# Performance work log

Measured on AMD Instinct MI355X. Metric: run time of the kernel, lower is better.

The kernel has to match this reference:

```python
import jax, jax.numpy as jnp
import numpy as np

HIDDEN = 1024
HEADS = 16
HEAD_DIM = HIDDEN // HEADS

def setup_inputs() -> dict:
    key = jax.random.key(0)
    ks = jax.random.split(key, 11)
    B, T, D = 2, 2048, HIDDEN
    s = 1.0 / np.sqrt(D)
    return {
        "query": jax.random.normal(ks[0], (B, T, D), jnp.float32),
        "key": jax.random.normal(ks[1], (B, T, D), jnp.float32),
        "value": jax.random.normal(ks[2], (B, T, D), jnp.float32),
        "Wq": jax.random.normal(ks[3], (D, D), jnp.float32) * s,
        "bq": jnp.zeros((D,), jnp.float32),
        "Wk": jax.random.normal(ks[4], (D, D), jnp.float32) * s,
        "bk": jnp.zeros((D,), jnp.float32),
        "Wv": jax.random.normal(ks[5], (D, D), jnp.float32) * s,
        "bv": jnp.zeros((D,), jnp.float32),
        "Wo": jax.random.normal(ks[6], (D, D), jnp.float32) * s,
        "bo": jnp.zeros((D,), jnp.float32),
    }

def reference(query, key, value, Wq, bq, Wk, bk, Wv, bv, Wo, bo):
    B, Tq, D = query.shape
    Tk = key.shape[1]
    H, Hd = HEADS, HEAD_DIM
    # projections -> [B, H, T, Hd]
    Q = (query @ Wq + bq).reshape(B, Tq, H, Hd).transpose(0, 2, 1, 3)
    K = (key @ Wk + bk).reshape(B, Tk, H, Hd).transpose(0, 2, 1, 3)
    V = (value @ Wv + bv).reshape(B, Tk, H, Hd).transpose(0, 2, 1, 3)
    scale = jnp.sqrt(jnp.asarray(Hd, Q.dtype))
    scores = jnp.einsum('bhqd,bhkd->bhqk', Q, K) / scale  # [B,H,Tq,Tk]
    causal = jnp.triu(jnp.ones((Tq, Tk), bool), k=1)
    scores = jnp.where(causal[None, None], jnp.asarray(-jnp.inf, scores.dtype), scores)
    attn = jax.nn.softmax(scores, axis=-1)
    out = jnp.einsum('bhqk,bhkd->bhqd', attn, V)  # [B,H,Tq,Hd]
    out = out.transpose(0, 2, 1, 3).reshape(B, Tq, D)
    return out @ Wo + bo
```

## Files before the change

kernel.cpp:

```cpp
#include <hip/hip_runtime.h>
#include <hip/hip_bf16.h>


typedef __bf16 bf16_t;
typedef __bf16 bf16x8 __attribute__((ext_vector_type(8)));
typedef __bf16 bf16x4 __attribute__((ext_vector_type(4)));
typedef __bf16 bf16x2 __attribute__((ext_vector_type(2)));
typedef short short4v __attribute__((ext_vector_type(4)));
typedef float f32x4 __attribute__((ext_vector_type(4)));
typedef unsigned int u32;

#define D_MODEL 1024
#define SEQ_T   2048
#define NHEAD   16
#define HDIM    64
#define M_ROWS  4096
#define MEGA    (1024 * 1024)

__device__ __forceinline__ void gl2lds16(const void* g, void* l) {
    __builtin_amdgcn_global_load_lds((const __attribute__((address_space(1))) u32*)g,
                                     (__attribute__((address_space(3))) u32*)l, 16, 0, 0);
}

__device__ __forceinline__ short4v as_s4(bf16x4 v) {
    union { bf16x4 h; short4v s; } u; u.h = v; return u.s;
}

__global__ __launch_bounds__(256) void prep(
    const float* __restrict__ Wq, const float* __restrict__ Wk,
    const float* __restrict__ Wv, const float* __restrict__ Wo,
    const float* __restrict__ Xq, const float* __restrict__ Xk, const float* __restrict__ Xv,
    bf16_t* __restrict__ Wqt, bf16_t* __restrict__ Wkt,
    bf16_t* __restrict__ Wvt, bf16_t* __restrict__ Wot,
    bf16_t* __restrict__ Xb)
{
    int blk = blockIdx.x, tid = threadIdx.x;
    if (blk < 1024) {
        int wi = blk >> 8, t = blk & 255;
        int n0 = (t & 15) * 64, k0 = (t >> 4) * 64;
        const float* W = wi == 0 ? Wq : (wi == 1 ? Wk : (wi == 2 ? Wv : Wo));
        bf16_t* Wt = wi == 0 ? Wqt : (wi == 1 ? Wkt : (wi == 2 ? Wvt : Wot));
        __shared__ float tile[64][65];
        int tx = tid & 63, ty = tid >> 6;
#pragma unroll
        for (int i = 0; i < 64; i += 4)
            tile[ty + i][tx] = W[(k0 + ty + i) * D_MODEL + n0 + tx];
        __syncthreads();
#pragma unroll
        for (int i = 0; i < 64; i += 4)
            Wt[(size_t)(n0 + ty + i) * D_MODEL + k0 + tx] = (bf16_t)tile[tx][ty + i];
    } else {
        int b2 = blk - 1024;
        int xi = b2 >> 9;
        const float* X = xi == 0 ? Xq : (xi == 1 ? Xk : Xv);
        bf16_t* XB = Xb + (size_t)xi * M_ROWS * D_MODEL;
        size_t base = (size_t)(b2 & 511) * 8192 + tid * 32;
#pragma unroll
        for (int half = 0; half < 2; half++) {
            const float4* xp = (const float4*)(X + base + half * 16);
            float4 a0 = xp[0], a1 = xp[1], a2 = xp[2], a3 = xp[3];
            bf16x8 o0, o1;
            o0[0] = (bf16_t)a0.x; o0[1] = (bf16_t)a0.y; o0[2] = (bf16_t)a0.z; o0[3] = (bf16_t)a0.w;
            o0[4] = (bf16_t)a1.x; o0[5] = (bf16_t)a1.y; o0[6] = (bf16_t)a1.z; o0[7] = (bf16_t)a1.w;
            o1[0] = (bf16_t)a2.x; o1[1] = (bf16_t)a2.y; o1[2] = (bf16_t)a2.z; o1[3] = (bf16_t)a2.w;
            o1[4] = (bf16_t)a3.x; o1[5] = (bf16_t)a3.y; o1[6] = (bf16_t)a3.z; o1[7] = (bf16_t)a3.w;
            *(bf16x8*)(XB + base + half * 16) = o0;
            *(bf16x8*)(XB + base + half * 16 + 8) = o1;
        }
    }
}

template <bool PRECAST>
__global__ __launch_bounds__(256) void proj_fused(
    const float* __restrict__ Xq, const float* __restrict__ Xk, const float* __restrict__ Xv,
    const bf16_t* __restrict__ Xb,
    const bf16_t* __restrict__ Wqt, const bf16_t* __restrict__ Wkt, const bf16_t* __restrict__ Wvt,
    const float* __restrict__ bq, const float* __restrict__ bk, const float* __restrict__ bv,
    bf16_t* __restrict__ Qh, bf16_t* __restrict__ Kh, bf16_t* __restrict__ Vt)
{
    __shared__ bf16_t Ab[128 * 32];
    __shared__ bf16_t Bb[128 * 32];
    int tid = threadIdx.x;
    int w = tid >> 6, lane = tid & 63, lo16 = lane & 15, quad = lane >> 4;
    int m0 = blockIdx.x * 128;
    int proj = blockIdx.y >> 3;
    int n0 = (blockIdx.y & 7) * 128;
    const float*  X    = proj == 0 ? Xq  : (proj == 1 ? Xk  : Xv);
    const bf16_t* XB   = Xb + (size_t)proj * M_ROWS * D_MODEL;
    const bf16_t* Wt   = proj == 0 ? Wqt : (proj == 1 ? Wkt : Wvt);
    const float*  bias = proj == 0 ? bq  : (proj == 1 ? bk  : bv);
    int wm = (w >> 1) * 64, wn = (w & 1) * 64;

    f32x4 acc[4][4];
#pragma unroll
    for (int i = 0; i < 4; i++)
#pragma unroll
        for (int j = 0; j < 4; j++) acc[i][j] = (f32x4){0.f, 0.f, 0.f, 0.f};

    for (int k0 = 0; k0 < D_MODEL; k0 += 32) {
        __syncthreads();
#pragma unroll
        for (int p = 0; p < 2; p++) {
            int idx = p * 256 + tid;
            int row = idx >> 2, cp = idx & 3, cl = (cp - row) & 3;
            if (PRECAST) {
                gl2lds16(XB + (size_t)(m0 + row) * D_MODEL + k0 + cl * 8, Ab + idx * 8);
            } else {
                const float* as = X + (size_t)(m0 + row) * D_MODEL + k0 + cl * 8;
                float4 a0 = *(const float4*)as, a1 = *(const float4*)(as + 4);
                bf16x8 av;
                av[0] = (bf16_t)a0.x; av[1] = (bf16_t)a0.y; av[2] = (bf16_t)a0.z; av[3] = (bf16_t)a0.w;
                av[4] = (bf16_t)a1.x; av[5] = (bf16_t)a1.y; av[6] = (bf16_t)a1.z; av[7] = (bf16_t)a1.w;
                *(bf16x8*)(Ab + idx * 8) = av;
            }
            gl2lds16(Wt + (size_t)(n0 + row) * D_MODEL + k0 + cl * 8, Bb + idx * 8);
        }
        __syncthreads();
        bf16x8 af[4], bfr[4];
#pragma unroll
        for (int i = 0; i < 4; i++) {
            int row = wm + i * 16 + lo16;
            af[i] = *(bf16x8*)(Ab + row * 32 + ((quad + row) & 3) * 8);
        }
#pragma unroll
        for (int j = 0; j < 4; j++) {
            int row = wn + j * 16 + lo16;
            bfr[j] = *(bf16x8*)(Bb + row * 32 + ((quad + row) & 3) * 8);
        }
#pragma unroll
        for (int i = 0; i < 4; i++)
#pragma unroll
            for (int j = 0; j < 4; j++)
                acc[i][j] = __builtin_amdgcn_mfma_f32_16x16x32_bf16(af[i], bfr[j], acc[i][j], 0, 0, 0);
    }

    float qscale = proj == 0 ? 0.125f : 1.0f;
#pragma unroll
    for (int j = 0; j < 4; j++) {
        int col = n0 + wn + j * 16 + lo16;
        float bv2 = bias[col];
        int h = col >> 6, hd = col & 63;
#pragma unroll
        for (int i = 0; i < 4; i++) {
#pragma unroll
            for (int r = 0; r < 4; r++) {
                int m = m0 + wm + i * 16 + quad * 4 + r;
                int b = m >> 11, t = m & 2047;
                bf16_t val = (bf16_t)((acc[i][j][r] + bv2) * qscale);
                if (proj == 2)
                    Vt[(((size_t)(b * NHEAD + h) * HDIM + hd) * SEQ_T) + t] = val;
                else if (proj == 1)
                    Kh[(((size_t)(b * NHEAD + h) * SEQ_T + t) * HDIM) + hd] = val;
                else
                    Qh[(((size_t)(b * NHEAD + h) * SEQ_T + t) * HDIM) + hd] = val;
            }
        }
    }
}

__global__ __launch_bounds__(256) void flash_attn(const bf16_t* __restrict__ Qh,
                                                  const bf16_t* __restrict__ Kh,
                                                  const bf16_t* __restrict__ Vt,
                                                  bf16_t* __restrict__ Ob) {
    int bh = blockIdx.x & 31;
    int pr = blockIdx.x >> 5;
    int tid = threadIdx.x;
    int w = tid >> 6, lane = tid & 63, lo16 = lane & 15, quad = lane >> 4;

    __shared__ bf16_t KL[2][64 * 64];
    __shared__ bf16_t VL[2][64 * 64];

    const bf16_t* Qp = Qh + (size_t)bh * SEQ_T * HDIM;
    const bf16_t* Kp = Kh + (size_t)bh * SEQ_T * HDIM;
    const bf16_t* Vp = Vt + (size_t)bh * HDIM * SEQ_T;
    int b = bh >> 4, h = bh & 15;

    auto stageKV = [&](int buf, int kt) {
#pragma unroll
        for (int p = 0; p < 2; p++) {
            int idx = p * 256 + tid;
            int row = idx >> 3, cp = idx & 7, cl = (cp - row) & 7;
            gl2lds16(Kp + (size_t)(kt * 64 + row) * HDIM + cl * 8, KL[buf] + idx * 8);
            gl2lds16(Vp + (size_t)row * SEQ_T + kt * 64 + cl * 8, VL[buf] + idx * 8);
        }
    };

    int qt_hi = 31 - pr, qt_lo = pr;
    int n0t = qt_hi + 1, ntot = n0t + qt_lo + 1;

    int qt_cur = qt_hi;
    int qbase = qt_cur * 64 + w * 16;
    bf16x8 qf0, qf1;
    f32x4 oacc[4];
    float lsum;

    auto load_q = [&]() {
        const bf16_t* qr = Qp + (size_t)(qbase + lo16) * HDIM;
        qf0 = *(const bf16x8*)(qr + quad * 8);
        qf1 = *(const bf16x8*)(qr + 32 + quad * 8);
    };
    auto zero_state = [&]() {
        lsum = 0.f;
#pragma unroll
        for (int t = 0; t < 4; t++) oacc[t] = (f32x4){0.f, 0.f, 0.f, 0.f};
    };
    auto epilogue = [&]() {
        float lt = lsum;
        lt += __shfl_xor(lt, 16);
        lt += __shfl_xor(lt, 32);
        float inv = 1.f / lt;
        int q = qbase + lo16;
        bf16_t* dst = Ob + ((size_t)b * SEQ_T + q) * D_MODEL + h * HDIM;
#pragma unroll
        for (int t = 0; t < 4; t++) {
#pragma unroll
            for (int rp = 0; rp < 2; rp++) {
                int d0 = t * 16 + quad * 4 + rp * 2;
                bf16x2 pk;
                pk[0] = (bf16_t)(oacc[t][rp * 2] * inv);
                pk[1] = (bf16_t)(oacc[t][rp * 2 + 1] * inv);
                *(bf16x2*)(dst + d0) = pk;
            }
        }
    };

    load_q();
    zero_state();
    stageKV(0, 0);
    __syncthreads();

    for (int j = 0; j < ntot; j++) {
        int cur = j & 1;
        if (j + 1 < ntot) {
            int jn = j + 1;
            int ktn = jn < n0t ? jn : jn - n0t;
            stageKV(jn & 1, ktn);
        }
        int kt = j < n0t ? j : j - n0t;

        bf16x8 kf[4][2];
#pragma unroll
        for (int s = 0; s < 4; s++) {
            int keyr = s * 16 + lo16;
            kf[s][0] = *(bf16x8*)(KL[cur] + keyr * 64 + ((quad + keyr) & 7) * 8);
            kf[s][1] = *(bf16x8*)(KL[cur] + keyr * 64 + ((quad + 4 + keyr) & 7) * 8);
        }

        f32x4 sacc[4];
#pragma unroll
        for (int s = 0; s < 4; s++) sacc[s] = (f32x4){0.f, 0.f, 0.f, 0.f};
#pragma unroll
        for (int s = 0; s < 4; s++) {
            sacc[s] = __builtin_amdgcn_mfma_f32_16x16x32_bf16(kf[s][0], qf0, sacc[s], 0, 0, 0);
            sacc[s] = __builtin_amdgcn_mfma_f32_16x16x32_bf16(kf[s][1], qf1, sacc[s], 0, 0, 0);
        }

        bool diag = (kt == qt_cur);
        int q = qbase + lo16;
        short4v pf[4];
#pragma unroll
        for (int s = 0; s < 4; s++) {
            bf16x4 pv;
#pragma unroll
            for (int r = 0; r < 4; r++) {
                float e = __expf(sacc[s][r]);
                if (diag) {
                    int key = kt * 64 + s * 16 + quad * 4 + r;
                    e = (key <= q) ? e : 0.f;
                }
                lsum += e;
                pv[r] = (bf16_t)e;
            }
            pf[s] = as_s4(pv);
        }

#pragma unroll
        for (int t = 0; t < 4; t++) {
            int drow = t * 16 + lo16;
#pragma unroll
            for (int s = 0; s < 4; s++) {
                int c = s * 16 + quad * 4;
                int phys = ((c >> 3) + drow) & 7;
                bf16x4 vf = *(bf16x4*)(VL[cur] + drow * 64 + phys * 8 + (c & 7));
                oacc[t] = __builtin_amdgcn_mfma_f32_16x16x16bf16_1k(as_s4(vf), pf[s], oacc[t], 0, 0, 0);
            }
        }

        __syncthreads();

        if (j == n0t - 1) {
            epilogue();
            qt_cur = qt_lo;
            qbase = qt_cur * 64 + w * 16;
            load_q();
            zero_state();
        }
    }
    epilogue();
}

__global__ __launch_bounds__(256) void out_gemm(const bf16_t* __restrict__ A,
                                                const bf16_t* __restrict__ Wt,
                                                const float* __restrict__ bias,
                                                float* __restrict__ out) {
    __shared__ bf16_t Ab[64 * 32];
    __shared__ bf16_t Bb[128 * 32];
    int tid = threadIdx.x;
    int w = tid >> 6, lane = tid & 63, lo16 = lane & 15, quad = lane >> 4;
    int m0 = blockIdx.x * 64;
    int n0 = blockIdx.y * 128;
    int wm = (w >> 1) * 32, wn = (w & 1) * 64;

    f32x4 acc[2][4];
#pragma unroll
    for (int i = 0; i < 2; i++)
#pragma unroll
        for (int j = 0; j < 4; j++) acc[i][j] = (f32x4){0.f, 0.f, 0.f, 0.f};

    for (int k0 = 0; k0 < D_MODEL; k0 += 32) {
        __syncthreads();
        {
            int idx = tid;
            int row = idx >> 2, cp = idx & 3, cl = (cp - row) & 3;
            gl2lds16(A + (size_t)(m0 + row) * D_MODEL + k0 + cl * 8, Ab + idx * 8);
        }
#pragma unroll
        for (int p = 0; p < 2; p++) {
            int idx = p * 256 + tid;
            int row = idx >> 2, cp = idx & 3, cl = (cp - row) & 3;
            gl2lds16(Wt + (size_t)(n0 + row) * D_MODEL + k0 + cl * 8, Bb + idx * 8);
        }
        __syncthreads();
        bf16x8 af[2], bfr[4];
#pragma unroll
        for (int i = 0; i < 2; i++) {
            int row = wm + i * 16 + lo16;
            af[i] = *(bf16x8*)(Ab + row * 32 + ((quad + row) & 3) * 8);
        }
#pragma unroll
        for (int j = 0; j < 4; j++) {
            int row = wn + j * 16 + lo16;
            bfr[j] = *(bf16x8*)(Bb + row * 32 + ((quad + row) & 3) * 8);
        }
#pragma unroll
        for (int i = 0; i < 2; i++)
#pragma unroll
            for (int j = 0; j < 4; j++)
                acc[i][j] = __builtin_amdgcn_mfma_f32_16x16x32_bf16(af[i], bfr[j], acc[i][j], 0, 0, 0);
    }

#pragma unroll
    for (int j = 0; j < 4; j++) {
        int col = n0 + wn + j * 16 + lo16;
        float bv2 = bias[col];
#pragma unroll
        for (int i = 0; i < 2; i++)
#pragma unroll
            for (int r = 0; r < 4; r++) {
                int m = m0 + wm + i * 16 + quad * 4 + r;
                out[(size_t)m * D_MODEL + col] = acc[i][j][r] + bv2;
            }
    }
}

extern "C" void kernel_launch(void* const* d_in, const int* in_sizes, int n_in,
                              void* d_out, int out_size, void* d_ws, size_t ws_size,
                              hipStream_t stream) {
    const float* q  = (const float*)d_in[0];
    const float* k  = (const float*)d_in[1];
    const float* v  = (const float*)d_in[2];
    const float* Wq = (const float*)d_in[3];
    const float* bq = (const float*)d_in[4];
    const float* Wk = (const float*)d_in[5];
    const float* bk = (const float*)d_in[6];
    const float* Wv = (const float*)d_in[7];
    const float* bv = (const float*)d_in[8];
    const float* Wo = (const float*)d_in[9];
    const float* bo = (const float*)d_in[10];
    float* out = (float*)d_out;

    bf16_t* Wqt = (bf16_t*)d_ws;
    bf16_t* Wkt = Wqt + (size_t)MEGA;
    bf16_t* Wvt = Wkt + (size_t)MEGA;
    bf16_t* Wot = Wvt + (size_t)MEGA;
    bf16_t* Qh  = Wot + (size_t)MEGA;
    bf16_t* Kh  = Qh  + (size_t)M_ROWS * D_MODEL;
    bf16_t* Vt  = Kh  + (size_t)M_ROWS * D_MODEL;
    bf16_t* Xb  = Vt  + (size_t)M_ROWS * D_MODEL;
    bf16_t* Ob  = Xb;

    bool precast = ws_size >= (size_t)(4 * MEGA + 6 * M_ROWS * D_MODEL) * sizeof(bf16_t);

    int prep_blocks = precast ? 1024 + 3 * 512 : 1024;
    prep<<<prep_blocks, 256, 0, stream>>>(Wq, Wk, Wv, Wo, q, k, v, Wqt, Wkt, Wvt, Wot, Xb);

    dim3 pg(M_ROWS / 128, 24);
    if (precast)
        proj_fused<true><<<pg, 256, 0, stream>>>(q, k, v, Xb, Wqt, Wkt, Wvt, bq, bk, bv, Qh, Kh, Vt);
    else
        proj_fused<false><<<pg, 256, 0, stream>>>(q, k, v, Xb, Wqt, Wkt, Wvt, bq, bk, bv, Qh, Kh, Vt);

    flash_attn<<<32 * 16, 256, 0, stream>>>(Qh, Kh, Vt, Ob);

    dim3 og(M_ROWS / 64, D_MODEL / 128);
    out_gemm<<<og, 256, 0, stream>>>(Ob, Wot, bo, out);
}
```

Before: 229.6 us.

## Split causal attention KV range across two blocks and merge partials in out-projection

The flash attention kernel no longer pairs a high and a low query tile in one block. It launches 2048 blocks, each covering one query tile and half of its causal KV range, and writes unnormalized bf16 partial outputs plus row sums to two buffers. The output GEMM sums the two partials and divides by the combined row sum while loading its A tile. The separate bf16 pre-cast of the activations is also dropped, so the projection GEMM always converts fp32 inputs inline. This trades more parallelism and shorter per-block chains for extra partial-output traffic, a non-async A-tile load in out_gemm, and a larger workspace requirement.

```diff
diff --git a/kernel.cpp b/kernel.cpp
--- a/kernel.cpp
+++ b/kernel.cpp
@@ -29,51 +29,27 @@
 __global__ __launch_bounds__(256) void prep(
     const float* __restrict__ Wq, const float* __restrict__ Wk,
     const float* __restrict__ Wv, const float* __restrict__ Wo,
-    const float* __restrict__ Xq, const float* __restrict__ Xk, const float* __restrict__ Xv,
     bf16_t* __restrict__ Wqt, bf16_t* __restrict__ Wkt,
-    bf16_t* __restrict__ Wvt, bf16_t* __restrict__ Wot,
-    bf16_t* __restrict__ Xb)
+    bf16_t* __restrict__ Wvt, bf16_t* __restrict__ Wot)
 {
     int blk = blockIdx.x, tid = threadIdx.x;
-    if (blk < 1024) {
-        int wi = blk >> 8, t = blk & 255;
-        int n0 = (t & 15) * 64, k0 = (t >> 4) * 64;
-        const float* W = wi == 0 ? Wq : (wi == 1 ? Wk : (wi == 2 ? Wv : Wo));
-        bf16_t* Wt = wi == 0 ? Wqt : (wi == 1 ? Wkt : (wi == 2 ? Wvt : Wot));
-        __shared__ float tile[64][65];
-        int tx = tid & 63, ty = tid >> 6;
-#pragma unroll
-        for (int i = 0; i < 64; i += 4)
-            tile[ty + i][tx] = W[(k0 + ty + i) * D_MODEL + n0 + tx];
-        __syncthreads();
-#pragma unroll
-        for (int i = 0; i < 64; i += 4)
-            Wt[(size_t)(n0 + ty + i) * D_MODEL + k0 + tx] = (bf16_t)tile[tx][ty + i];
-    } else {
-        int b2 = blk - 1024;
-        int xi = b2 >> 9;
-        const float* X = xi == 0 ? Xq : (xi == 1 ? Xk : Xv);
-        bf16_t* XB = Xb + (size_t)xi * M_ROWS * D_MODEL;
-        size_t base = (size_t)(b2 & 511) * 8192 + tid * 32;
-#pragma unroll
-        for (int half = 0; half < 2; half++) {
-            const float4* xp = (const float4*)(X + base + half * 16);
-            float4 a0 = xp[0], a1 = xp[1], a2 = xp[2], a3 = xp[3];
-            bf16x8 o0, o1;
-            o0[0] = (bf16_t)a0.x; o0[1] = (bf16_t)a0.y; o0[2] = (bf16_t)a0.z; o0[3] = (bf16_t)a0.w;
-            o0[4] = (bf16_t)a1.x; o0[5] = (bf16_t)a1.y; o0[6] = (bf16_t)a1.z; o0[7] = (bf16_t)a1.w;
-            o1[0] = (bf16_t)a2.x; o1[1] = (bf16_t)a2.y; o1[2] = (bf16_t)a2.z; o1[3] = (bf16_t)a2.w;
-            o1[4] = (bf16_t)a3.x; o1[5] = (bf16_t)a3.y; o1[6] = (bf16_t)a3.z; o1[7] = (bf16_t)a3.w;
-            *(bf16x8*)(XB + base + half * 16) = o0;
-            *(bf16x8*)(XB + base + half * 16 + 8) = o1;
-        }
-    }
-}
-
-template <bool PRECAST>
+    int wi = blk >> 8, t = blk & 255;
+    int n0 = (t & 15) * 64, k0 = (t >> 4) * 64;
+    const float* W = wi == 0 ? Wq : (wi == 1 ? Wk : (wi == 2 ? Wv : Wo));
+    bf16_t* Wt = wi == 0 ? Wqt : (wi == 1 ? Wkt : (wi == 2 ? Wvt : Wot));
+    __shared__ float tile[64][65];
+    int tx = tid & 63, ty = tid >> 6;
+#pragma unroll
+    for (int i = 0; i < 64; i += 4)
+        tile[ty + i][tx] = W[(k0 + ty + i) * D_MODEL + n0 + tx];
+    __syncthreads();
+#pragma unroll
+    for (int i = 0; i < 64; i += 4)
+        Wt[(size_t)(n0 + ty + i) * D_MODEL + k0 + tx] = (bf16_t)tile[tx][ty + i];
+}
+
 __global__ __launch_bounds__(256) void proj_fused(
     const float* __restrict__ Xq, const float* __restrict__ Xk, const float* __restrict__ Xv,
-    const bf16_t* __restrict__ Xb,
     const bf16_t* __restrict__ Wqt, const bf16_t* __restrict__ Wkt, const bf16_t* __restrict__ Wvt,
     const float* __restrict__ bq, const float* __restrict__ bk, const float* __restrict__ bv,
     bf16_t* __restrict__ Qh, bf16_t* __restrict__ Kh, bf16_t* __restrict__ Vt)
@@ -86,7 +62,6 @@
     int proj = blockIdx.y >> 3;
     int n0 = (blockIdx.y & 7) * 128;
     const float*  X    = proj == 0 ? Xq  : (proj == 1 ? Xk  : Xv);
-    const bf16_t* XB   = Xb + (size_t)proj * M_ROWS * D_MODEL;
     const bf16_t* Wt   = proj == 0 ? Wqt : (proj == 1 ? Wkt : Wvt);
     const float*  bias = proj == 0 ? bq  : (proj == 1 ? bk  : bv);
     int wm = (w >> 1) * 64, wn = (w & 1) * 64;
@@ -103,16 +78,12 @@
         for (int p = 0; p < 2; p++) {
             int idx = p * 256 + tid;
             int row = idx >> 2, cp = idx & 3, cl = (cp - row) & 3;
-            if (PRECAST) {
-                gl2lds16(XB + (size_t)(m0 + row) * D_MODEL + k0 + cl * 8, Ab + idx * 8);
-            } else {
-                const float* as = X + (size_t)(m0 + row) * D_MODEL + k0 + cl * 8;
-                float4 a0 = *(const float4*)as, a1 = *(const float4*)(as + 4);
-                bf16x8 av;
-                av[0] = (bf16_t)a0.x; av[1] = (bf16_t)a0.y; av[2] = (bf16_t)a0.z; av[3] = (bf16_t)a0.w;
-                av[4] = (bf16_t)a1.x; av[5] = (bf16_t)a1.y; av[6] = (bf16_t)a1.z; av[7] = (bf16_t)a1.w;
-                *(bf16x8*)(Ab + idx * 8) = av;
-            }
+            const float* as = X + (size_t)(m0 + row) * D_MODEL + k0 + cl * 8;
+            float4 a0 = *(const float4*)as, a1 = *(const float4*)(as + 4);
+            bf16x8 av;
+            av[0] = (bf16_t)a0.x; av[1] = (bf16_t)a0.y; av[2] = (bf16_t)a0.z; av[3] = (bf16_t)a0.w;
+            av[4] = (bf16_t)a1.x; av[5] = (bf16_t)a1.y; av[6] = (bf16_t)a1.z; av[7] = (bf16_t)a1.w;
+            *(bf16x8*)(Ab + idx * 8) = av;
             gl2lds16(Wt + (size_t)(n0 + row) * D_MODEL + k0 + cl * 8, Bb + idx * 8);
         }
         __syncthreads();
@@ -161,9 +132,14 @@
 __global__ __launch_bounds__(256) void flash_attn(const bf16_t* __restrict__ Qh,
                                                   const bf16_t* __restrict__ Kh,
                                                   const bf16_t* __restrict__ Vt,
-                                                  bf16_t* __restrict__ Ob) {
-    int bh = blockIdx.x & 31;
-    int pr = blockIdx.x >> 5;
+                                                  bf16_t* __restrict__ Op0,
+                                                  bf16_t* __restrict__ Op1,
+                                                  float* __restrict__ L0,
+                                                  float* __restrict__ L1) {
+    int bi = blockIdx.x;
+    int qt = 31 - (bi >> 6);
+    int half = (bi >> 5) & 1;
+    int bh = bi & 31;
     int tid = threadIdx.x;
     int w = tid >> 6, lane = tid & 63, lo16 = lane & 15, quad = lane >> 4;
 
@@ -174,6 +150,26 @@
     const bf16_t* Kp = Kh + (size_t)bh * SEQ_T * HDIM;
     const bf16_t* Vp = Vt + (size_t)bh * HDIM * SEQ_T;
     int b = bh >> 4, h = bh & 15;
+
+    bf16_t* Op = half ? Op1 : Op0;
+    float*  L  = half ? L1 : L0;
+
+    int nt = qt + 1;
+    int mid = (nt + 1) >> 1;
+    int kt0 = half ? mid : 0;
+    int kt1 = half ? nt  : mid;
+
+    int qbase = qt * 64 + w * 16;
+    int qrow = qbase + lo16;
+
+    const bf16_t* qr = Qp + (size_t)qrow * HDIM;
+    bf16x8 qf0 = *(const bf16x8*)(qr + quad * 8);
+    bf16x8 qf1 = *(const bf16x8*)(qr + 32 + quad * 8);
+
+    f32x4 oacc[4];
+#pragma unroll
+    for (int t = 0; t < 4; t++) oacc[t] = (f32x4){0.f, 0.f, 0.f, 0.f};
+    float lsum = 0.f;
 
     auto stageKV = [&](int buf, int kt) {
 #pragma unroll
@@ -185,121 +181,87 @@
         }
     };
 
-    int qt_hi = 31 - pr, qt_lo = pr;
-    int n0t = qt_hi + 1, ntot = n0t + qt_lo + 1;
-
-    int qt_cur = qt_hi;
-    int qbase = qt_cur * 64 + w * 16;
-    bf16x8 qf0, qf1;
-    f32x4 oacc[4];
-    float lsum;
-
-    auto load_q = [&]() {
-        const bf16_t* qr = Qp + (size_t)(qbase + lo16) * HDIM;
-        qf0 = *(const bf16x8*)(qr + quad * 8);
-        qf1 = *(const bf16x8*)(qr + 32 + quad * 8);
-    };
-    auto zero_state = [&]() {
-        lsum = 0.f;
-#pragma unroll
-        for (int t = 0; t < 4; t++) oacc[t] = (f32x4){0.f, 0.f, 0.f, 0.f};
-    };
-    auto epilogue = [&]() {
-        float lt = lsum;
-        lt += __shfl_xor(lt, 16);
-        lt += __shfl_xor(lt, 32);
-        float inv = 1.f / lt;
-        int q = qbase + lo16;
-        bf16_t* dst = Ob + ((size_t)b * SEQ_T + q) * D_MODEL + h * HDIM;
-#pragma unroll
-        for (int t = 0; t < 4; t++) {
-#pragma unroll
-            for (int rp = 0; rp < 2; rp++) {
-                int d0 = t * 16 + quad * 4 + rp * 2;
-                bf16x2 pk;
-                pk[0] = (bf16_t)(oacc[t][rp * 2] * inv);
-                pk[1] = (bf16_t)(oacc[t][rp * 2 + 1] * inv);
-                *(bf16x2*)(dst + d0) = pk;
-            }
-        }
-    };
-
-    load_q();
-    zero_state();
-    stageKV(0, 0);
-    __syncthreads();
-
-    for (int j = 0; j < ntot; j++) {
-        int cur = j & 1;
-        if (j + 1 < ntot) {
-            int jn = j + 1;
-            int ktn = jn < n0t ? jn : jn - n0t;
-            stageKV(jn & 1, ktn);
-        }
-        int kt = j < n0t ? j : j - n0t;
-
-        bf16x8 kf[4][2];
-#pragma unroll
-        for (int s = 0; s < 4; s++) {
-            int keyr = s * 16 + lo16;
-            kf[s][0] = *(bf16x8*)(KL[cur] + keyr * 64 + ((quad + keyr) & 7) * 8);
-            kf[s][1] = *(bf16x8*)(KL[cur] + keyr * 64 + ((quad + 4 + keyr) & 7) * 8);
-        }
-
-        f32x4 sacc[4];
-#pragma unroll
-        for (int s = 0; s < 4; s++) sacc[s] = (f32x4){0.f, 0.f, 0.f, 0.f};
-#pragma unroll
-        for (int s = 0; s < 4; s++) {
-            sacc[s] = __builtin_amdgcn_mfma_f32_16x16x32_bf16(kf[s][0], qf0, sacc[s], 0, 0, 0);
-            sacc[s] = __builtin_amdgcn_mfma_f32_16x16x32_bf16(kf[s][1], qf1, sacc[s], 0, 0, 0);
-        }
-
-        bool diag = (kt == qt_cur);
-        int q = qbase + lo16;
-        short4v pf[4];
-#pragma unroll
-        for (int s = 0; s < 4; s++) {
-            bf16x4 pv;
-#pragma unroll
-            for (int r = 0; r < 4; r++) {
-                float e = __expf(sacc[s][r]);
-                if (diag) {
-                    int key = kt * 64 + s * 16 + quad * 4 + r;
-                    e = (key <= q) ? e : 0.f;
+    if (kt0 < kt1) {
+        stageKV(0, kt0);
+        __syncthreads();
+        for (int j = kt0; j < kt1; j++) {
+            int cur = (j - kt0) & 1;
+            if (j + 1 < kt1) stageKV(cur ^ 1, j + 1);
+
+            bf16x8 kf[4][2];
+#pragma unroll
+            for (int s = 0; s < 4; s++) {
+                int keyr = s * 16 + lo16;
+                kf[s][0] = *(bf16x8*)(KL[cur] + keyr * 64 + ((quad + keyr) & 7) * 8);
+                kf[s][1] = *(bf16x8*)(KL[cur] + keyr * 64 + ((quad + 4 + keyr) & 7) * 8);
+            }
+
+            f32x4 sacc[4];
+#pragma unroll
+            for (int s = 0; s < 4; s++) sacc[s] = (f32x4){0.f, 0.f, 0.f, 0.f};
+#pragma unroll
+            for (int s = 0; s < 4; s++) {
+                sacc[s] = __builtin_amdgcn_mfma_f32_16x16x32_bf16(kf[s][0], qf0, sacc[s], 0, 0, 0);
+                sacc[s] = __builtin_amdgcn_mfma_f32_16x16x32_bf16(kf[s][1], qf1, sacc[s], 0, 0, 0);
+            }
+
+            bool diag = (j == qt);
+            short4v pf[4];
+#pragma unroll
+            for (int s = 0; s < 4; s++) {
+                bf16x4 pv;
+#pragma unroll
+                for (int r = 0; r < 4; r++) {
+                    float e = __expf(sacc[s][r]);
+                    if (diag) {
+                        int key = j * 64 + s * 16 + quad * 4 + r;
+                        e = (key <= qrow) ? e : 0.f;
+                    }
+                    lsum += e;
+                    pv[r] = (bf16_t)e;
                 }
-                lsum += e;
-                pv[r] = (bf16_t)e;
-            }
-            pf[s] = as_s4(pv);
-        }
-
-#pragma unroll
-        for (int t = 0; t < 4; t++) {
-            int drow = t * 16 + lo16;
-#pragma unroll
-            for (int s = 0; s < 4; s++) {
-                int c = s * 16 + quad * 4;
-                int phys = ((c >> 3) + drow) & 7;
-                bf16x4 vf = *(bf16x4*)(VL[cur] + drow * 64 + phys * 8 + (c & 7));
-                oacc[t] = __builtin_amdgcn_mfma_f32_16x16x16bf16_1k(as_s4(vf), pf[s], oacc[t], 0, 0, 0);
-            }
-        }
-
-        __syncthreads();
-
-        if (j == n0t - 1) {
-            epilogue();
-            qt_cur = qt_lo;
-            qbase = qt_cur * 64 + w * 16;
-            load_q();
-            zero_state();
-        }
-    }
-    epilogue();
-}
-
-__global__ __launch_bounds__(256) void out_gemm(const bf16_t* __restrict__ A,
+                pf[s] = as_s4(pv);
+            }
+
+#pragma unroll
+            for (int t = 0; t < 4; t++) {
+                int drow = t * 16 + lo16;
+#pragma unroll
+                for (int s = 0; s < 4; s++) {
+                    int c = s * 16 + quad * 4;
+                    int phys = ((c >> 3) + drow) & 7;
+                    bf16x4 vf = *(bf16x4*)(VL[cur] + drow * 64 + phys * 8 + (c & 7));
+                    oacc[t] = __builtin_amdgcn_mfma_f32_16x16x16bf16_1k(as_s4(vf), pf[s], oacc[t], 0, 0, 0);
+                }
+            }
+
+            __syncthreads();
+        }
+    }
+
+    float lt = lsum;
+    lt += __shfl_xor(lt, 16);
+    lt += __shfl_xor(lt, 32);
+    bf16_t* dst = Op + ((size_t)b * SEQ_T + qrow) * D_MODEL + h * HDIM;
+#pragma unroll
+    for (int t = 0; t < 4; t++) {
+#pragma unroll
+        for (int rp = 0; rp < 2; rp++) {
+            int d0 = t * 16 + quad * 4 + rp * 2;
+            bf16x2 pk;
+            pk[0] = (bf16_t)oacc[t][rp * 2];
+            pk[1] = (bf16_t)oacc[t][rp * 2 + 1];
+            *(bf16x2*)(dst + d0) = pk;
+        }
+    }
+    if (quad == 0)
+        L[((size_t)b * SEQ_T + qrow) * NHEAD + h] = lt;
+}
+
+__global__ __launch_bounds__(256) void out_gemm(const bf16_t* __restrict__ Op0,
+                                                const bf16_t* __restrict__ Op1,
+                                                const float* __restrict__ L0,
+                                                const float* __restrict__ L1,
                                                 const bf16_t* __restrict__ Wt,
                                                 const float* __restrict__ bias,
                                                 float* __restrict__ out) {
@@ -322,7 +284,17 @@
         {
             int idx = tid;
             int row = idx >> 2, cp = idx & 3, cl = (cp - row) & 3;
-            gl2lds16(A + (size_t)(m0 + row) * D_MODEL + k0 + cl * 8, Ab + idx * 8);
+            int gr = m0 + row;
+            int c0 = k0 + cl * 8;
+            int hidx = gr * NHEAD + (c0 >> 6);
+            float inv = 1.f / (L0[hidx] + L1[hidx]);
+            bf16x8 a0 = *(const bf16x8*)(Op0 + (size_t)gr * D_MODEL + c0);
+            bf16x8 a1 = *(const bf16x8*)(Op1 + (size_t)gr * D_MODEL + c0);
+            bf16x8 av;
+#pragma unroll
+            for (int e = 0; e < 8; e++)
+                av[e] = (bf16_t)(((float)a0[e] + (float)a1[e]) * inv);
+            *(bf16x8*)(Ab + idx * 8) = av;
         }
 #pragma unroll
         for (int p = 0; p < 2; p++) {
@@ -386,22 +358,18 @@
     bf16_t* Qh  = Wot + (size_t)MEGA;
     bf16_t* Kh  = Qh  + (size_t)M_ROWS * D_MODEL;
     bf16_t* Vt  = Kh  + (size_t)M_ROWS * D_MODEL;
-    bf16_t* Xb  = Vt  + (size_t)M_ROWS * D_MODEL;
-    bf16_t* Ob  = Xb;
-
-    bool precast = ws_size >= (size_t)(4 * MEGA + 6 * M_ROWS * D_MODEL) * sizeof(bf16_t);
-
-    int prep_blocks = precast ? 1024 + 3 * 512 : 1024;
-    prep<<<prep_blocks, 256, 0, stream>>>(Wq, Wk, Wv, Wo, q, k, v, Wqt, Wkt, Wvt, Wot, Xb);
+    bf16_t* Op0 = Vt  + (size_t)M_ROWS * D_MODEL;
+    bf16_t* Op1 = Op0 + (size_t)M_ROWS * D_MODEL;
+    float*  L0  = (float*)(Op1 + (size_t)M_ROWS * D_MODEL);
+    float*  L1  = L0 + (size_t)M_ROWS * NHEAD;
+
+    prep<<<1024, 256, 0, stream>>>(Wq, Wk, Wv, Wo, Wqt, Wkt, Wvt, Wot);
 
     dim3 pg(M_ROWS / 128, 24);
-    if (precast)
-        proj_fused<true><<<pg, 256, 0, stream>>>(q, k, v, Xb, Wqt, Wkt, Wvt, bq, bk, bv, Qh, Kh, Vt);
-    else
-        proj_fused<false><<<pg, 256, 0, stream>>>(q, k, v, Xb, Wqt, Wkt, Wvt, bq, bk, bv, Qh, Kh, Vt);
-
-    flash_attn<<<32 * 16, 256, 0, stream>>>(Qh, Kh, Vt, Ob);
+    proj_fused<<<pg, 256, 0, stream>>>(q, k, v, Wqt, Wkt, Wvt, bq, bk, bv, Qh, Kh, Vt);
+
+    flash_attn<<<2048, 256, 0, stream>>>(Qh, Kh, Vt, Op0, Op1, L0, L1);
 
     dim3 og(M_ROWS / 64, D_MODEL / 128);
-    out_gemm<<<og, 256, 0, stream>>>(Ob, Wot, bo, out);
-}
+    out_gemm<<<og, 256, 0, stream>>>(Op0, Op1, L0, L1, Wot, bo, out);
+}
```

After: 233.7 us. Within noise of the previous version (+1.8%).
